# Kernel optimization log

Hardware: AMD Instinct MI355X
Metric: run time of the kernel (lower is better)

Reference implementation:

```python
import jax, jax.numpy as jnp
import numpy as np

D_MODEL = 1024
N_HEADS = 16
D_HEAD = D_MODEL // N_HEADS
B, L = 2, 2048


def setup_inputs() -> dict:
    key = jax.random.key(0)
    ks = jax.random.split(key, 12)
    s = 1.0 / np.sqrt(D_MODEL)
    inp = {
        "q": jax.random.normal(ks[0], (B, L, D_MODEL), jnp.float32),
        "k": jax.random.normal(ks[1], (B, L, D_MODEL), jnp.float32),
        "v": jax.random.normal(ks[2], (B, L, D_MODEL), jnp.float32),
        "Wq": jax.random.uniform(ks[3], (D_MODEL, D_MODEL), jnp.float32, -s, s),
        "bq": jax.random.uniform(ks[4], (D_MODEL,), jnp.float32, -s, s),
        "Wk": jax.random.uniform(ks[5], (D_MODEL, D_MODEL), jnp.float32, -s, s),
        "bk": jax.random.uniform(ks[6], (D_MODEL,), jnp.float32, -s, s),
        "Wv": jax.random.uniform(ks[7], (D_MODEL, D_MODEL), jnp.float32, -s, s),
        "bv": jax.random.uniform(ks[8], (D_MODEL,), jnp.float32, -s, s),
        "Wo": jax.random.uniform(ks[9], (D_MODEL, D_MODEL), jnp.float32, -s, s),
        "bo": jax.random.uniform(ks[10], (D_MODEL,), jnp.float32, -s, s),
        # causal mask: True = masked out (matches torch masked_fill semantics)
        "attn_mask": jnp.triu(jnp.ones((L, L), jnp.bool_), k=1),
    }
    return inp


def reference(q, k, v, Wq, bq, Wk, bk, Wv, bv, Wo, bo, attn_mask):
    Bz, Lq, D = q.shape
    def split_heads(x):
        return x.reshape(x.shape[0], x.shape[1], N_HEADS, D_HEAD).transpose(0, 2, 1, 3)
    Q = split_heads(q @ Wq.T + bq)  # [B,H,L,Dh]
    K = split_heads(k @ Wk.T + bk)
    V = split_heads(v @ Wv.T + bv)
    scores = jnp.einsum("bhqd,bhkd->bhqk", Q, K) / jnp.sqrt(jnp.float32(D_HEAD))
    scores = jnp.where(attn_mask[None, None, :, :], -jnp.inf, scores)
    attn = jax.nn.softmax(scores, axis=-1)
    # dropout is identity in eval / p=0
    out_heads = jnp.einsum("bhqk,bhkd->bhqd", attn, V)
    out = out_heads.transpose(0, 2, 1, 3).reshape(Bz, Lq, D)
    return out @ Wo.T + bo
```

## Files before the change

### kernel.cpp

```cpp
#include <hip/hip_runtime.h>
#include <hip/hip_bf16.h>
#include <stdint.h>

typedef __attribute__((ext_vector_type(8))) short bf16x8;
typedef __attribute__((ext_vector_type(4))) float f32x4;

#define DEV static __device__ __forceinline__

constexpr int DM = 1024;
constexpr int LQ = 2048;
constexpr int NB = 2;
constexpr int NHD = 16;
constexpr int DH = 64;
constexpr int MT = NB * LQ;

constexpr float SCL2 = 0.125f * 1.4426950408889634f;

DEV unsigned short f2bf(float f) {
  union { float f; unsigned u; } x; x.f = f;
  unsigned r = x.u + 0x7fffu + ((x.u >> 16) & 1u);
  return (unsigned short)(r >> 16);
}
DEV float bf2f(short s) {
  union { unsigned u; float f; } x; x.u = ((unsigned)(unsigned short)s) << 16;
  return x.f;
}
DEV unsigned packtrunc(float a, float b) {
  union { float f; unsigned u; } x, y; x.f = a; y.f = b;
  return (x.u >> 16) | (y.u & 0xffff0000u);
}
DEV f32x4 MFMA(bf16x8 a, bf16x8 b, f32x4 c) {
  return __builtin_amdgcn_mfma_f32_16x16x32_bf16(a, b, c, 0, 0, 0);
}
DEV void gld16(const void* g, void* l) {
  __builtin_amdgcn_global_load_lds(
      (const __attribute__((address_space(1))) unsigned int*)g,
      (__attribute__((address_space(3))) unsigned int*)l, 16, 0, 0);
}

DEV void cvt_body(const float* __restrict__ in, unsigned short* __restrict__ out) {
  long i = ((long)blockIdx.x * blockDim.x + threadIdx.x) * 8;
  f32x4 a = *(const f32x4*)(in + i);
  f32x4 b = *(const f32x4*)(in + i + 4);
  bf16x8 r;
#pragma unroll
  for (int e = 0; e < 4; ++e) {
    r[e]     = (short)f2bf(a[e]);
    r[e + 4] = (short)f2bf(b[e]);
  }
  *(bf16x8*)(out + i) = r;
}

__global__ void cvt3(const float* __restrict__ a, const float* __restrict__ b,
                     const float* __restrict__ c,
                     unsigned short* oa, unsigned short* ob, unsigned short* oc) {
  const float* src = blockIdx.y == 0 ? a : blockIdx.y == 1 ? b : c;
  unsigned short* dst = blockIdx.y == 0 ? oa : blockIdx.y == 1 ? ob : oc;
  cvt_body(src, dst);
}

__global__ void cvt4(const float* __restrict__ a, const float* __restrict__ b,
                     const float* __restrict__ c, const float* __restrict__ d,
                     unsigned short* oa, unsigned short* ob,
                     unsigned short* oc, unsigned short* od) {
  const float* src = blockIdx.y == 0 ? a : blockIdx.y == 1 ? b
                   : blockIdx.y == 2 ? c : d;
  unsigned short* dst = blockIdx.y == 0 ? oa : blockIdx.y == 1 ? ob
                      : blockIdx.y == 2 ? oc : od;
  cvt_body(src, dst);
}

template<int BN, int MODE>
DEV void gemm_body(short* As, short* Bs,
                   const unsigned short* __restrict__ A,
                   const unsigned short* __restrict__ W,
                   const float* __restrict__ bias,
                   void* __restrict__ outp) {
  constexpr int K = DM, N = DM;
  constexpr int MI = (BN == 128) ? 4 : 2;
  const int tid = threadIdx.x;
  const int lane = tid & 63, wave = tid >> 6;
  const int g = lane >> 4, c = lane & 15;
  const int wr = (BN == 128) ? (wave >> 1) : wave;
  const int wc = (BN == 128) ? (wave & 1) : 0;
  const long m0 = (long)blockIdx.y * 128, n0 = (long)blockIdx.x * BN;
  const int sr = lane >> 2, sc = (lane & 3) * 8;

  f32x4 acc[MI][4] = {};

  for (int ks = 0; ks < K / 32; ++ks) {
    const int k0 = ks * 32;
    __syncthreads();
#pragma unroll
    for (int u = 0; u < 2; ++u) {
      const int ci = wave * 2 + u;
      gld16(A + (m0 + ci * 16 + sr) * K + k0 + sc, As + ci * 512);
      if (BN == 128)
        gld16(W + (n0 + ci * 16 + sr) * K + k0 + sc, Bs + ci * 512);
    }
    if (BN == 64)
      gld16(W + (n0 + wave * 16 + sr) * K + k0 + sc, Bs + wave * 512);
    __syncthreads();

    bf16x8 af[MI], bfr[4];
#pragma unroll
    for (int i = 0; i < MI; ++i)
      af[i] = *(const bf16x8*)(As + (wr * (MI * 16) + i * 16 + c) * 32 + g * 8);
#pragma unroll
    for (int j = 0; j < 4; ++j)
      bfr[j] = *(const bf16x8*)(Bs + (wc * 64 + j * 16 + c) * 32 + g * 8);
#pragma unroll
    for (int i = 0; i < MI; ++i)
#pragma unroll
      for (int j = 0; j < 4; ++j)
        acc[i][j] = MFMA(af[i], bfr[j], acc[i][j]);
  }

#pragma unroll
  for (int i = 0; i < MI; ++i) {
#pragma unroll
    for (int j = 0; j < 4; ++j) {
      const int n = (int)n0 + wc * 64 + j * 16 + c;
      const float bv = bias[n];
#pragma unroll
      for (int r = 0; r < 4; ++r) {
        const int m = (int)m0 + wr * (MI * 16) + i * 16 + g * 4 + r;
        const float val = acc[i][j][r] + bv;
        if (MODE == 0) {
          ((unsigned short*)outp)[(long)m * N + n] = f2bf(val);
        } else if (MODE == 1) {
          const int b = m >> 11, l = m & 2047;
          const int h = n >> 6, d = n & 63;
          ((unsigned short*)outp)[(((long)(b * NHD + h)) * DH + d) * LQ + l] =
              f2bf(val);
        } else {
          ((float*)outp)[(long)m * N + n] = val;
        }
      }
    }
  }
}

__global__ __launch_bounds__(256, 3)
void qkv_proj(const unsigned short* __restrict__ QB,
              const unsigned short* __restrict__ KB,
              const unsigned short* __restrict__ VB,
              const unsigned short* __restrict__ WQb,
              const unsigned short* __restrict__ WKb,
              const unsigned short* __restrict__ WVb,
              const float* __restrict__ bq, const float* __restrict__ bk,
              const float* __restrict__ bv,
              unsigned short* QP, unsigned short* KP, unsigned short* VT) {
  __shared__ short As[128 * 32];
  __shared__ short Bs[128 * 32];
  const int z = blockIdx.z;
  if (z == 0)      gemm_body<128, 0>(As, Bs, QB, WQb, bq, QP);
  else if (z == 1) gemm_body<128, 0>(As, Bs, KB, WKb, bk, KP);
  else             gemm_body<128, 1>(As, Bs, VB, WVb, bv, VT);
}

__global__ __launch_bounds__(256, 2)
void oproj(const unsigned short* __restrict__ A,
           const unsigned short* __restrict__ W,
           const float* __restrict__ bias, float* out) {
  __shared__ short As[128 * 32];
  __shared__ short Bs[64 * 32];
  gemm_body<64, 2>(As, Bs, A, W, bias, out);
}

template<bool DIAG>
DEV void attn_qtile(const bf16x8 kf[4][2], const bf16x8 vf[4][2],
                    const bf16x8* qf, short (*ps)[72],
                    float& mrow, float& lsum, f32x4* oacc,
                    int g, int c, int qrow, int kv0) {
  f32x4 sacc[4] = {};
#pragma unroll
  for (int jt = 0; jt < 4; ++jt) {
    sacc[jt] = MFMA(kf[jt][0], qf[0], sacc[jt]);
    sacc[jt] = MFMA(kf[jt][1], qf[1], sacc[jt]);
  }
  float s2[4][4];
  float rmax = -1e30f;
#pragma unroll
  for (int jt = 0; jt < 4; ++jt)
#pragma unroll
    for (int r = 0; r < 4; ++r) {
      float s = sacc[jt][r];
      if (DIAG) {
        const int kvi = kv0 + jt * 16 + 4 * g + r;
        s = (kvi <= qrow) ? s : -1e30f;
      }
      s2[jt][r] = s;
      rmax = fmaxf(rmax, s);
    }
  rmax = fmaxf(rmax, __shfl_xor(rmax, 16, 64));
  rmax = fmaxf(rmax, __shfl_xor(rmax, 32, 64));
  const float mnew = fmaxf(mrow, rmax);
  const float scl = __builtin_amdgcn_exp2f(mrow - mnew);
  mrow = mnew;
  float rsum = 0.f;
#pragma unroll
  for (int jt = 0; jt < 4; ++jt) {
    const float p0 = __builtin_amdgcn_exp2f(s2[jt][0] - mnew);
    const float p1 = __builtin_amdgcn_exp2f(s2[jt][1] - mnew);
    const float p2 = __builtin_amdgcn_exp2f(s2[jt][2] - mnew);
    const float p3 = __builtin_amdgcn_exp2f(s2[jt][3] - mnew);
    rsum += (p0 + p1) + (p2 + p3);
    uint2 w;
    w.x = packtrunc(p0, p1);
    w.y = packtrunc(p2, p3);
    *(uint2*)&ps[c][jt * 16 + 4 * g] = w;
  }
  rsum += __shfl_xor(rsum, 16, 64);
  rsum += __shfl_xor(rsum, 32, 64);
  lsum = lsum * scl + rsum;

  float sclr[4];
#pragma unroll
  for (int r = 0; r < 4; ++r) sclr[r] = __shfl(scl, 4 * g + r, 64);
#pragma unroll
  for (int dj = 0; dj < 4; ++dj)
#pragma unroll
    for (int r = 0; r < 4; ++r) oacc[dj][r] *= sclr[r];

  const bf16x8 pf0 = *(const bf16x8*)&ps[c][g * 8];
  const bf16x8 pf1 = *(const bf16x8*)&ps[c][32 + g * 8];
#pragma unroll
  for (int dj = 0; dj < 4; ++dj) {
    oacc[dj] = MFMA(pf0, vf[dj][0], oacc[dj]);
    oacc[dj] = MFMA(pf1, vf[dj][1], oacc[dj]);
  }
}

__global__ __launch_bounds__(256, 2)
void attn5(const unsigned short* __restrict__ Qp,
           const unsigned short* __restrict__ Kp,
           const unsigned short* __restrict__ Vt,
           unsigned short* __restrict__ Ob) {
  __shared__ short Ks[2][64][72];
  __shared__ short Vs[2][64][72];
  __shared__ short Ps[64][72];
  const int tid = threadIdx.x;
  const int lane = tid & 63, wave = tid >> 6;
  const int g = lane >> 4, c = lane & 15;
  const int qbA = blockIdx.x;
  const int bh = blockIdx.y;
  const int b = bh >> 4, hd = bh & 15;
  const int jmax = 31 - qbA;
  const int q0A = qbA * 64 + wave * 16;
  const int q0B = jmax * 64 + wave * 16;

  const unsigned short* Qbase = Qp + (long)b * LQ * DM + hd * DH;
  const unsigned short* Kbase = Kp + (long)b * LQ * DM + hd * DH;
  const unsigned short* Vbase = Vt + (long)bh * DH * LQ;

  bf16x8 qfA[2], qfB[2];
#pragma unroll
  for (int h = 0; h < 2; ++h) {
    bf16x8 tA = *(const bf16x8*)(Qbase + (long)(q0A + c) * DM + h * 32 + g * 8);
    bf16x8 tB = *(const bf16x8*)(Qbase + (long)(q0B + c) * DM + h * 32 + g * 8);
#pragma unroll
    for (int e = 0; e < 8; ++e) {
      tA[e] = (short)f2bf(bf2f(tA[e]) * SCL2);
      tB[e] = (short)f2bf(bf2f(tB[e]) * SCL2);
    }
    qfA[h] = tA;
    qfB[h] = tB;
  }

  const int srow = tid >> 3;
  const int scol = (tid & 7) * 8;
  bf16x8 kr0, kr1, vr0, vr1;

#define LOAD_TILE(J)                                                         \
  {                                                                          \
    const unsigned short* kp_ = Kbase + (long)((J) * 64 + srow) * DM + scol; \
    kr0 = *(const bf16x8*)kp_;                                               \
    kr1 = *(const bf16x8*)(kp_ + 32 * DM);                                   \
    const unsigned short* vp_ = Vbase + (long)srow * LQ + (J) * 64 + scol;   \
    vr0 = *(const bf16x8*)vp_;                                               \
    vr1 = *(const bf16x8*)(vp_ + 32 * LQ);                                   \
  }
#define WRITE_TILE(BUF)                                                      \
  {                                                                          \
    *(bf16x8*)&Ks[BUF][srow][scol]      = kr0;                               \
    *(bf16x8*)&Ks[BUF][srow + 32][scol] = kr1;                               \
    *(bf16x8*)&Vs[BUF][srow][scol]      = vr0;                               \
    *(bf16x8*)&Vs[BUF][srow + 32][scol] = vr1;                               \
  }

  LOAD_TILE(0);
  WRITE_TILE(0);
  LOAD_TILE(1);
  __syncthreads();

  float mA = -1e30f, lA = 0.f, mB = -1e30f, lB = 0.f;
  f32x4 oA[4] = {}, oB[4] = {};
  short (*ps)[72] = (short(*)[72])&Ps[wave * 16][0];

  for (int j = 0; j <= jmax; ++j) {
    const int cur = j & 1;
    if (j < jmax) WRITE_TILE(cur ^ 1);
    if (j + 2 <= jmax) LOAD_TILE(j + 2);

    bf16x8 kf[4][2], vf[4][2];
#pragma unroll
    for (int jt = 0; jt < 4; ++jt) {
      kf[jt][0] = *(const bf16x8*)&Ks[cur][jt * 16 + c][g * 8];
      kf[jt][1] = *(const bf16x8*)&Ks[cur][jt * 16 + c][32 + g * 8];
      vf[jt][0] = *(const bf16x8*)&Vs[cur][jt * 16 + c][g * 8];
      vf[jt][1] = *(const bf16x8*)&Vs[cur][jt * 16 + c][32 + g * 8];
    }

    if (j < qbA)
      attn_qtile<false>(kf, vf, qfA, ps, mA, lA, oA, g, c, q0A + c, j * 64);
    else if (j == qbA)
      attn_qtile<true>(kf, vf, qfA, ps, mA, lA, oA, g, c, q0A + c, j * 64);

    if (j < jmax)
      attn_qtile<false>(kf, vf, qfB, ps, mB, lB, oB, g, c, q0B + c, j * 64);
    else
      attn_qtile<true>(kf, vf, qfB, ps, mB, lB, oB, g, c, q0B + c, j * 64);

    __syncthreads();
  }
#undef LOAD_TILE
#undef WRITE_TILE

#pragma unroll
  for (int it = 0; it < 2; ++it) {
    f32x4* oacc = it ? oB : oA;
    const float lsum = it ? lB : lA;
    const int q0 = it ? q0B : q0A;
#pragma unroll
    for (int r = 0; r < 4; ++r) {
      const float ls = __shfl(lsum, 4 * g + r, 64);
      const float inv = 1.0f / ls;
      const int q = q0 + 4 * g + r;
#pragma unroll
      for (int dj = 0; dj < 4; ++dj)
        Ob[((long)b * LQ + q) * DM + hd * DH + dj * 16 + c] =
            f2bf(oacc[dj][r] * inv);
    }
  }
}

extern "C" void kernel_launch(void* const* d_in, const int* in_sizes, int n_in,
                              void* d_out, int out_size, void* d_ws, size_t ws_size,
                              hipStream_t stream) {
  const float* q  = (const float*)d_in[0];
  const float* k  = (const float*)d_in[1];
  const float* v  = (const float*)d_in[2];
  const float* Wq = (const float*)d_in[3];
  const float* bq = (const float*)d_in[4];
  const float* Wk = (const float*)d_in[5];
  const float* bk = (const float*)d_in[6];
  const float* Wv = (const float*)d_in[7];
  const float* bv = (const float*)d_in[8];
  const float* Wo = (const float*)d_in[9];
  const float* bo = (const float*)d_in[10];

  unsigned short* ws = (unsigned short*)d_ws;
  const long NQKV = (long)MT * DM;
  const long NW   = (long)DM * DM;
  unsigned short* QB  = ws;
  unsigned short* KB  = QB + NQKV;
  unsigned short* VB  = KB + NQKV;
  unsigned short* WQb = VB + NQKV;
  unsigned short* WKb = WQb + NW;
  unsigned short* WVb = WKb + NW;
  unsigned short* WOb = WVb + NW;
  unsigned short* QP  = WOb + NW;
  unsigned short* KP  = QP + NQKV;
  unsigned short* VT  = KP + NQKV;
  unsigned short* OB  = QB;

  cvt3<<<dim3((int)(NQKV / 2048), 3), 256, 0, stream>>>(q, k, v, QB, KB, VB);
  cvt4<<<dim3((int)(NW / 2048), 4), 256, 0, stream>>>(Wq, Wk, Wv, Wo,
                                                      WQb, WKb, WVb, WOb);

  qkv_proj<<<dim3(8, 32, 3), 256, 0, stream>>>(QB, KB, VB, WQb, WKb, WVb,
                                               bq, bk, bv, QP, KP, VT);

  attn5<<<dim3(16, 32), 256, 0, stream>>>(QP, KP, VT, OB);

  oproj<<<dim3(16, 32), 256, 0, stream>>>(OB, WOb, bo, (float*)d_out);
}
```

Baseline: 132.5 us.

## Double GEMM K-step to 64 and interleave QK MFMAs for both attention q-tiles

The projection GEMMs now load a 64-wide K slice per iteration as two 32-wide halves, which halves the number of barrier pairs and gives each sync twice as many MFMAs. Shared memory doubles, and the qkv launch bound drops from 3 to 2 blocks per CU. In attention, the QK score MFMAs for both paired q-tiles are issued before either softmax, with a separate P buffer per tile, so matrix work can overlap softmax latency. V fragments are loaded after the QK step. Register pressure rises from the extra fragments and the second score accumulator.

```diff
diff --git a/kernel.cpp b/kernel.cpp
--- a/kernel.cpp
+++ b/kernel.cpp
@@ -78,6 +78,7 @@
                    void* __restrict__ outp) {
   constexpr int K = DM, N = DM;
   constexpr int MI = (BN == 128) ? 4 : 2;
+  constexpr int BH = BN * 32;
   const int tid = threadIdx.x;
   const int lane = tid & 63, wave = tid >> 6;
   const int g = lane >> 4, c = lane & 15;
@@ -88,32 +89,51 @@
 
   f32x4 acc[MI][4] = {};
 
-  for (int ks = 0; ks < K / 32; ++ks) {
-    const int k0 = ks * 32;
+  for (int ks = 0; ks < K / 64; ++ks) {
+    const int k0 = ks * 64;
     __syncthreads();
 #pragma unroll
-    for (int u = 0; u < 2; ++u) {
-      const int ci = wave * 2 + u;
-      gld16(A + (m0 + ci * 16 + sr) * K + k0 + sc, As + ci * 512);
-      if (BN == 128)
-        gld16(W + (n0 + ci * 16 + sr) * K + k0 + sc, Bs + ci * 512);
-    }
-    if (BN == 64)
-      gld16(W + (n0 + wave * 16 + sr) * K + k0 + sc, Bs + wave * 512);
+    for (int h = 0; h < 2; ++h) {
+#pragma unroll
+      for (int u = 0; u < 2; ++u) {
+        const int ci = wave * 2 + u;
+        gld16(A + (m0 + ci * 16 + sr) * K + k0 + h * 32 + sc,
+              As + h * 4096 + ci * 512);
+      }
+      if (BN == 128) {
+#pragma unroll
+        for (int u = 0; u < 2; ++u) {
+          const int ci = wave * 2 + u;
+          gld16(W + (n0 + ci * 16 + sr) * K + k0 + h * 32 + sc,
+                Bs + h * BH + ci * 512);
+        }
+      } else {
+        gld16(W + (n0 + wave * 16 + sr) * K + k0 + h * 32 + sc,
+              Bs + h * BH + wave * 512);
+      }
+    }
     __syncthreads();
 
-    bf16x8 af[MI], bfr[4];
+    bf16x8 af[MI][2], bfr[4][2];
 #pragma unroll
     for (int i = 0; i < MI; ++i)
-      af[i] = *(const bf16x8*)(As + (wr * (MI * 16) + i * 16 + c) * 32 + g * 8);
+#pragma unroll
+      for (int h = 0; h < 2; ++h)
+        af[i][h] = *(const bf16x8*)(As + h * 4096 +
+                                    (wr * (MI * 16) + i * 16 + c) * 32 + g * 8);
 #pragma unroll
     for (int j = 0; j < 4; ++j)
-      bfr[j] = *(const bf16x8*)(Bs + (wc * 64 + j * 16 + c) * 32 + g * 8);
+#pragma unroll
+      for (int h = 0; h < 2; ++h)
+        bfr[j][h] = *(const bf16x8*)(Bs + h * BH +
+                                     (wc * 64 + j * 16 + c) * 32 + g * 8);
 #pragma unroll
     for (int i = 0; i < MI; ++i)
 #pragma unroll
-      for (int j = 0; j < 4; ++j)
-        acc[i][j] = MFMA(af[i], bfr[j], acc[i][j]);
+      for (int j = 0; j < 4; ++j) {
+        acc[i][j] = MFMA(af[i][0], bfr[j][0], acc[i][j]);
+        acc[i][j] = MFMA(af[i][1], bfr[j][1], acc[i][j]);
+      }
   }
 
 #pragma unroll
@@ -141,7 +161,7 @@
   }
 }
 
-__global__ __launch_bounds__(256, 3)
+__global__ __launch_bounds__(256, 2)
 void qkv_proj(const unsigned short* __restrict__ QB,
               const unsigned short* __restrict__ KB,
               const unsigned short* __restrict__ VB,
@@ -151,8 +171,8 @@
               const float* __restrict__ bq, const float* __restrict__ bk,
               const float* __restrict__ bv,
               unsigned short* QP, unsigned short* KP, unsigned short* VT) {
-  __shared__ short As[128 * 32];
-  __shared__ short Bs[128 * 32];
+  __shared__ short As[2 * 128 * 32];
+  __shared__ short Bs[2 * 128 * 32];
   const int z = blockIdx.z;
   if (z == 0)      gemm_body<128, 0>(As, Bs, QB, WQb, bq, QP);
   else if (z == 1) gemm_body<128, 0>(As, Bs, KB, WKb, bk, KP);
@@ -163,22 +183,23 @@
 void oproj(const unsigned short* __restrict__ A,
            const unsigned short* __restrict__ W,
            const float* __restrict__ bias, float* out) {
-  __shared__ short As[128 * 32];
-  __shared__ short Bs[64 * 32];
+  __shared__ short As[2 * 128 * 32];
+  __shared__ short Bs[2 * 64 * 32];
   gemm_body<64, 2>(As, Bs, A, W, bias, out);
 }
 
-template<bool DIAG>
-DEV void attn_qtile(const bf16x8 kf[4][2], const bf16x8 vf[4][2],
-                    const bf16x8* qf, short (*ps)[72],
-                    float& mrow, float& lsum, f32x4* oacc,
-                    int g, int c, int qrow, int kv0) {
-  f32x4 sacc[4] = {};
+DEV void qk8(const bf16x8 kf[4][2], const bf16x8* qf, f32x4* sacc) {
 #pragma unroll
   for (int jt = 0; jt < 4; ++jt) {
     sacc[jt] = MFMA(kf[jt][0], qf[0], sacc[jt]);
     sacc[jt] = MFMA(kf[jt][1], qf[1], sacc[jt]);
   }
+}
+
+template<bool DIAG>
+DEV void sm_pv(f32x4* sacc, const bf16x8 vf[4][2], short (*ps)[72],
+               float& mrow, float& lsum, f32x4* oacc,
+               int g, int c, int qrow, int kv0) {
   float s2[4][4];
   float rmax = -1e30f;
 #pragma unroll
@@ -233,13 +254,13 @@
 }
 
 __global__ __launch_bounds__(256, 2)
-void attn5(const unsigned short* __restrict__ Qp,
+void attn8(const unsigned short* __restrict__ Qp,
            const unsigned short* __restrict__ Kp,
            const unsigned short* __restrict__ Vt,
            unsigned short* __restrict__ Ob) {
   __shared__ short Ks[2][64][72];
   __shared__ short Vs[2][64][72];
-  __shared__ short Ps[64][72];
+  __shared__ short Ps[2][64][72];
   const int tid = threadIdx.x;
   const int lane = tid & 63, wave = tid >> 6;
   const int g = lane >> 4, c = lane & 15;
@@ -296,31 +317,42 @@
 
   float mA = -1e30f, lA = 0.f, mB = -1e30f, lB = 0.f;
   f32x4 oA[4] = {}, oB[4] = {};
-  short (*ps)[72] = (short(*)[72])&Ps[wave * 16][0];
+  short (*psA)[72] = (short(*)[72])&Ps[0][wave * 16][0];
+  short (*psB)[72] = (short(*)[72])&Ps[1][wave * 16][0];
+  const int qrowA = q0A + c, qrowB = q0B + c;
 
   for (int j = 0; j <= jmax; ++j) {
     const int cur = j & 1;
     if (j < jmax) WRITE_TILE(cur ^ 1);
     if (j + 2 <= jmax) LOAD_TILE(j + 2);
 
-    bf16x8 kf[4][2], vf[4][2];
+    bf16x8 kf[4][2];
 #pragma unroll
     for (int jt = 0; jt < 4; ++jt) {
       kf[jt][0] = *(const bf16x8*)&Ks[cur][jt * 16 + c][g * 8];
       kf[jt][1] = *(const bf16x8*)&Ks[cur][jt * 16 + c][32 + g * 8];
+    }
+
+    f32x4 sA[4] = {}, sB[4] = {};
+    if (j <= qbA) qk8(kf, qfA, sA);
+    qk8(kf, qfB, sB);
+
+    bf16x8 vf[4][2];
+#pragma unroll
+    for (int jt = 0; jt < 4; ++jt) {
       vf[jt][0] = *(const bf16x8*)&Vs[cur][jt * 16 + c][g * 8];
       vf[jt][1] = *(const bf16x8*)&Vs[cur][jt * 16 + c][32 + g * 8];
     }
 
     if (j < qbA)
-      attn_qtile<false>(kf, vf, qfA, ps, mA, lA, oA, g, c, q0A + c, j * 64);
+      sm_pv<false>(sA, vf, psA, mA, lA, oA, g, c, qrowA, j * 64);
     else if (j == qbA)
-      attn_qtile<true>(kf, vf, qfA, ps, mA, lA, oA, g, c, q0A + c, j * 64);
+      sm_pv<true>(sA, vf, psA, mA, lA, oA, g, c, qrowA, j * 64);
 
     if (j < jmax)
-      attn_qtile<false>(kf, vf, qfB, ps, mB, lB, oB, g, c, q0B + c, j * 64);
+      sm_pv<false>(sB, vf, psB, mB, lB, oB, g, c, qrowB, j * 64);
     else
-      attn_qtile<true>(kf, vf, qfB, ps, mB, lB, oB, g, c, q0B + c, j * 64);
+      sm_pv<true>(sB, vf, psB, mB, lB, oB, g, c, qrowB, j * 64);
 
     __syncthreads();
   }
@@ -382,7 +414,7 @@
   qkv_proj<<<dim3(8, 32, 3), 256, 0, stream>>>(QB, KB, VB, WQb, WKb, WVb,
                                                bq, bk, bv, QP, KP, VT);
 
-  attn5<<<dim3(16, 32), 256, 0, stream>>>(QP, KP, VT, OB);
+  attn8<<<dim3(16, 32), 256, 0, stream>>>(QP, KP, VT, OB);
 
   oproj<<<dim3(16, 32), 256, 0, stream>>>(OB, WOb, bo, (float*)d_out);
 }
```

New measurement: 128.4 us. -3.1%, faster.
